# Performance work log

Hardware: AMD Instinct MI355X
Metric: run time of the kernel (lower is better)

Reference implementation:

```python
import jax, jax.numpy as jnp
import numpy as np

R = 4  # search_range

def setup_inputs() -> dict:
    key = jax.random.key(0)
    k1, k2 = jax.random.split(key)
    B, C, H, W = 4, 128, 96, 160
    src = jax.random.normal(k1, (B, C, H, W), dtype=jnp.float32)
    tgt = jax.random.normal(k2, (B, C, H, W), dtype=jnp.float32)
    return {"src": src, "tgt": tgt}

def _cost_volume(src, tgt):
    B, C, H, W = src.shape
    # zero-pad tgt by R on each spatial side (as in F.pad(tgt, [R]*4))
    tp = jnp.pad(tgt, ((0, 0), (0, 0), (R, R), (R, R)))
    # shifted map cropped to the central HxW window; shift (dh, dw) means
    # the neighbor at offset (dh, dw) relative to each src pixel.
    def crop(dh, dw):
        return tp[:, :, R + dh:R + dh + H, R + dw:R + dw + W]
    # order matches torch: [identity, left, right, up, down] for i=1..R
    maps = [crop(0, 0)]
    for i in range(1, R + 1):
        maps.extend([crop(-i, 0), crop(i, 0), crop(0, -i), crop(0, i)])
    neigh = jnp.stack(maps, axis=2)  # [B, C, 1+4R, H, W]
    # correlation: sum over channels -> [B, 1+4R, H, W]
    return jnp.einsum('bchw,bcshw->bshw', src, neigh)

def reference(src, tgt):
    return _cost_volume(src, tgt)
```

## Files before the change

kernel.cpp:

```cpp
#include <hip/hip_runtime.h>

#define RR 4
#define NS 17
#define BB 4
#define CC 128
#define HH 96
#define WW 160
#define HWSZ (HH * WW)

#define TW 32
#define HTILE 8
#define TROWS (HTILE + 2 * RR)
#define TCOLS (TW + 2 * RR)
#define TILE_E (TROWS * TCOLS)
#define CCHUNK 32
#define NCHUNK (CC / CCHUNK)
#define CG 4
#define NG (CCHUNK / CG)
#define NSPX (WW / TW)
#define NSPY (HH / HTILE)
#define NSP (NSPX * NSPY)
#define NWG (NSP * BB * NCHUNK)
#define NXCD 8
#define WGPX (NWG / NXCD)

#define FMA4(a, t) \
    (a) = fmaf(svx, (t).x, fmaf(svy, (t).y, fmaf(svz, (t).z, fmaf(svw, (t).w, (a)))))

__global__ __launch_bounds__(256, 4)
void cost_volume_kernel(const float* __restrict__ src,
                        const float* __restrict__ tgt,
                        float* __restrict__ out) {
    __shared__ float4 tile[TILE_E];

    const int x   = threadIdx.x;
    const int hg  = threadIdx.y;
    const int tid = hg * TW + x;

    const int flat = blockIdx.x;
    const int wg   = (flat & (NXCD - 1)) * WGPX + (flat >> 3);
    const int sp   = wg % NSP;
    const int z    = wg / NSP;
    const int wx   = sp % NSPX;
    const int wy   = sp / NSPX;

    const int w0 = wx * TW;
    const int h0 = wy * HTILE;
    const int b  = z & 3;
    const int c0 = (z >> 2) * CCHUNK;

    const int w = w0 + x;
    const int h = h0 + hg;

    const float* tgt_b = tgt + (size_t)(b * CC + c0) * HWSZ;
    const float* src_p = src + (size_t)(b * CC + c0) * HWSZ + h * WW + w;

    int  sOff[3];
    bool sVal[3];
#pragma unroll
    for (int k = 0; k < 3; ++k) {
        const int idx = tid + k * 256;
        const int r   = idx / TCOLS;
        const int col = idx - r * TCOLS;
        const int gr  = h0 - RR + r;
        const int gc  = w0 - RR + col;
        sVal[k] = (idx < TILE_E) && gr >= 0 && gr < HH && gc >= 0 && gc < WW;
        sOff[k] = gr * WW + gc;
    }

    float4 pre[3];
    float  sv4[4];

    auto fetch = [&](int g) {
        const float* t = tgt_b + (size_t)(g * CG) * HWSZ;
#pragma unroll
        for (int k = 0; k < 3; ++k) {
            float4 v = make_float4(0.f, 0.f, 0.f, 0.f);
            if (sVal[k]) {
                const float* p = t + sOff[k];
                v.x = p[0];
                v.y = p[HWSZ];
                v.z = p[2 * HWSZ];
                v.w = p[3 * HWSZ];
            }
            pre[k] = v;
        }
        const float* s = src_p + (size_t)(g * CG) * HWSZ;
#pragma unroll
        for (int k = 0; k < 4; ++k) sv4[k] = s[k * HWSZ];
    };

    float acc[NS];
#pragma unroll
    for (int s = 0; s < NS; ++s) acc[s] = 0.f;

    fetch(0);
    const int base = (RR + hg) * TCOLS + (RR + x);

    for (int g = 0; g < NG; ++g) {
        tile[tid]       = pre[0];
        tile[tid + 256] = pre[1];
        if (tid + 512 < TILE_E) tile[tid + 512] = pre[2];
        const float svx = sv4[0], svy = sv4[1], svz = sv4[2], svw = sv4[3];
        __syncthreads();

        if (g + 1 < NG) fetch(g + 1);

        {
            float4 tc = tile[base];
            FMA4(acc[0], tc);
#pragma unroll
            for (int off = 1; off <= RR; ++off) {
                float4 tu = tile[base - off * TCOLS];
                float4 td = tile[base + off * TCOLS];
                float4 tl = tile[base - off];
                float4 tr = tile[base + off];
                FMA4(acc[4 * off - 3], tu);
                FMA4(acc[4 * off - 2], td);
                FMA4(acc[4 * off - 1], tl);
                FMA4(acc[4 * off    ], tr);
            }
        }
        __syncthreads();
    }

    float* op = out + (((size_t)b * NS) * HH + h) * WW + w;
#pragma unroll
    for (int s = 0; s < NS; ++s) {
        atomicAdd(op + (size_t)s * HWSZ, acc[s]);
    }
}

extern "C" void kernel_launch(void* const* d_in, const int* in_sizes, int n_in,
                              void* d_out, int out_size, void* d_ws, size_t ws_size,
                              hipStream_t stream) {
    const float* src = (const float*)d_in[0];
    const float* tgt = (const float*)d_in[1];
    float* out = (float*)d_out;

    hipMemsetAsync(out, 0, (size_t)out_size * sizeof(float), stream);

    dim3 block(TW, 8, 1);
    dim3 grid(NWG, 1, 1);
    cost_volume_kernel<<<grid, block, 0, stream>>>(src, tgt, out);
}
```

Before: 107.4 us.

## Double-buffer shared tile and halve channel chunk for more workgroups

Switches the shared-memory tile to two buffers, so each channel group needs one barrier instead of two. The next group is stored into the alternate buffer after compute, and the loop is fully unrolled. The channel chunk per workgroup drops from 32 to 16, which doubles the grid and the number of atomic adds to the output. The launch-bounds occupancy hint rises to 6. Doubling LDS per block and adding atomic traffic may offset the gains in parallelism and synchronisation.

```diff
diff --git a/kernel.cpp b/kernel.cpp
--- a/kernel.cpp
+++ b/kernel.cpp
@@ -13,7 +13,7 @@
 #define TROWS (HTILE + 2 * RR)
 #define TCOLS (TW + 2 * RR)
 #define TILE_E (TROWS * TCOLS)
-#define CCHUNK 32
+#define CCHUNK 16
 #define NCHUNK (CC / CCHUNK)
 #define CG 4
 #define NG (CCHUNK / CG)
@@ -27,11 +27,11 @@
 #define FMA4(a, t) \
     (a) = fmaf(svx, (t).x, fmaf(svy, (t).y, fmaf(svz, (t).z, fmaf(svw, (t).w, (a)))))
 
-__global__ __launch_bounds__(256, 4)
+__global__ __launch_bounds__(256, 6)
 void cost_volume_kernel(const float* __restrict__ src,
                         const float* __restrict__ tgt,
                         float* __restrict__ out) {
-    __shared__ float4 tile[TILE_E];
+    __shared__ float4 tile[2][TILE_E];
 
     const int x   = threadIdx.x;
     const int hg  = threadIdx.y;
@@ -69,9 +69,10 @@
     }
 
     float4 pre[3];
-    float  sv4[4];
+    float  svc[4];
+    float  svn[4];
 
-    auto fetch = [&](int g) {
+    auto fetch = [&](int g, float sv[4]) {
         const float* t = tgt_b + (size_t)(g * CG) * HWSZ;
 #pragma unroll
         for (int k = 0; k < 3; ++k) {
@@ -87,41 +88,55 @@
         }
         const float* s = src_p + (size_t)(g * CG) * HWSZ;
 #pragma unroll
-        for (int k = 0; k < 4; ++k) sv4[k] = s[k * HWSZ];
+        for (int k = 0; k < 4; ++k) sv[k] = s[k * HWSZ];
+    };
+
+    auto store_tile = [&](int buf) {
+        tile[buf][tid]       = pre[0];
+        tile[buf][tid + 256] = pre[1];
+        if (tid + 512 < TILE_E) tile[buf][tid + 512] = pre[2];
     };
 
     float acc[NS];
 #pragma unroll
     for (int s = 0; s < NS; ++s) acc[s] = 0.f;
 
-    fetch(0);
+    fetch(0, svc);
+    store_tile(0);
+    __syncthreads();
+
     const int base = (RR + hg) * TCOLS + (RR + x);
 
+#pragma unroll
     for (int g = 0; g < NG; ++g) {
-        tile[tid]       = pre[0];
-        tile[tid + 256] = pre[1];
-        if (tid + 512 < TILE_E) tile[tid + 512] = pre[2];
-        const float svx = sv4[0], svy = sv4[1], svz = sv4[2], svw = sv4[3];
-        __syncthreads();
+        const int cur = g & 1;
 
-        if (g + 1 < NG) fetch(g + 1);
+        if (g + 1 < NG) fetch(g + 1, svn);
 
         {
-            float4 tc = tile[base];
+            const float svx = svc[0], svy = svc[1], svz = svc[2], svw = svc[3];
+            const float4* tb = tile[cur];
+            float4 tc = tb[base];
             FMA4(acc[0], tc);
 #pragma unroll
             for (int off = 1; off <= RR; ++off) {
-                float4 tu = tile[base - off * TCOLS];
-                float4 td = tile[base + off * TCOLS];
-                float4 tl = tile[base - off];
-                float4 tr = tile[base + off];
+                float4 tu = tb[base - off * TCOLS];
+                float4 td = tb[base + off * TCOLS];
+                float4 tl = tb[base - off];
+                float4 tr = tb[base + off];
                 FMA4(acc[4 * off - 3], tu);
                 FMA4(acc[4 * off - 2], td);
                 FMA4(acc[4 * off - 1], tl);
                 FMA4(acc[4 * off    ], tr);
             }
         }
-        __syncthreads();
+
+        if (g + 1 < NG) {
+            store_tile(cur ^ 1);
+#pragma unroll
+            for (int k = 0; k < 4; ++k) svc[k] = svn[k];
+            __syncthreads();
+        }
     }
 
     float* op = out + (((size_t)b * NS) * HH + h) * WW + w;
```

Result: slower. 243.7 us (+126.9%).

## Compute two output rows per thread to reuse vertical tile loads

Applied to the files above, without the earlier changes.

Each thread now computes two vertically adjacent output pixels, doubling the tile height to 16 rows. The shared-memory column of ten float4 values is loaded once and feeds both rows' vertical-shift accumulators, which cuts LDS reads per output and shrinks the halo overhead relative to the tile. The XCD-aware block remapping is replaced by a channel-major linear ordering. The cost is twice as many accumulator registers, which may pressure occupancy under the 4-waves launch bound, and half as many workgroups.

```diff
diff --git a/kernel.cpp b/kernel.cpp
--- a/kernel.cpp
+++ b/kernel.cpp
@@ -9,7 +9,8 @@
 #define HWSZ (HH * WW)
 
 #define TW 32
-#define HTILE 8
+#define HTILE 16
+#define TH 2
 #define TROWS (HTILE + 2 * RR)
 #define TCOLS (TW + 2 * RR)
 #define TILE_E (TROWS * TCOLS)
@@ -21,11 +22,9 @@
 #define NSPY (HH / HTILE)
 #define NSP (NSPX * NSPY)
 #define NWG (NSP * BB * NCHUNK)
-#define NXCD 8
-#define WGPX (NWG / NXCD)
 
-#define FMA4(a, t) \
-    (a) = fmaf(svx, (t).x, fmaf(svy, (t).y, fmaf(svz, (t).z, fmaf(svw, (t).w, (a)))))
+#define FMA4S(a, t, s0, s1, s2, s3) \
+    (a) = fmaf((s0), (t).x, fmaf((s1), (t).y, fmaf((s2), (t).z, fmaf((s3), (t).w, (a)))))
 
 __global__ __launch_bounds__(256, 4)
 void cost_volume_kernel(const float* __restrict__ src,
@@ -38,27 +37,27 @@
     const int tid = hg * TW + x;
 
     const int flat = blockIdx.x;
-    const int wg   = (flat & (NXCD - 1)) * WGPX + (flat >> 3);
-    const int sp   = wg % NSP;
-    const int z    = wg / NSP;
-    const int wx   = sp % NSPX;
-    const int wy   = sp / NSPX;
+    const int ch   = flat / 120;
+    const int rr_  = flat % 120;
+    const int b    = rr_ / NSP;
+    const int spl  = rr_ % NSP;
+    const int wx   = spl % NSPX;
+    const int wy   = spl / NSPX;
 
+    const int c0 = ch * CCHUNK;
     const int w0 = wx * TW;
     const int h0 = wy * HTILE;
-    const int b  = z & 3;
-    const int c0 = (z >> 2) * CCHUNK;
 
-    const int w = w0 + x;
-    const int h = h0 + hg;
+    const int w  = w0 + x;
+    const int hb = h0 + hg * TH;
 
     const float* tgt_b = tgt + (size_t)(b * CC + c0) * HWSZ;
-    const float* src_p = src + (size_t)(b * CC + c0) * HWSZ + h * WW + w;
+    const float* src_p = src + (size_t)(b * CC + c0) * HWSZ + hb * WW + w;
 
-    int  sOff[3];
-    bool sVal[3];
+    int  sOff[4];
+    bool sVal[4];
 #pragma unroll
-    for (int k = 0; k < 3; ++k) {
+    for (int k = 0; k < 4; ++k) {
         const int idx = tid + k * 256;
         const int r   = idx / TCOLS;
         const int col = idx - r * TCOLS;
@@ -68,13 +67,13 @@
         sOff[k] = gr * WW + gc;
     }
 
-    float4 pre[3];
-    float  sv4[4];
+    float4 pre[4];
+    float  sv[2][4];
 
     auto fetch = [&](int g) {
         const float* t = tgt_b + (size_t)(g * CG) * HWSZ;
 #pragma unroll
-        for (int k = 0; k < 3; ++k) {
+        for (int k = 0; k < 4; ++k) {
             float4 v = make_float4(0.f, 0.f, 0.f, 0.f);
             if (sVal[k]) {
                 const float* p = t + sOff[k];
@@ -87,47 +86,64 @@
         }
         const float* s = src_p + (size_t)(g * CG) * HWSZ;
 #pragma unroll
-        for (int k = 0; k < 4; ++k) sv4[k] = s[k * HWSZ];
+        for (int k = 0; k < 4; ++k) {
+            sv[0][k] = s[k * HWSZ];
+            sv[1][k] = s[k * HWSZ + WW];
+        }
     };
 
-    float acc[NS];
+    float acc0[NS], acc1[NS];
 #pragma unroll
-    for (int s = 0; s < NS; ++s) acc[s] = 0.f;
+    for (int s = 0; s < NS; ++s) { acc0[s] = 0.f; acc1[s] = 0.f; }
 
     fetch(0);
-    const int base = (RR + hg) * TCOLS + (RR + x);
+    const int tr0 = RR + hg * TH;
+    const int cc  = RR + x;
 
     for (int g = 0; g < NG; ++g) {
         tile[tid]       = pre[0];
         tile[tid + 256] = pre[1];
-        if (tid + 512 < TILE_E) tile[tid + 512] = pre[2];
-        const float svx = sv4[0], svy = sv4[1], svz = sv4[2], svw = sv4[3];
+        tile[tid + 512] = pre[2];
+        if (tid < TILE_E - 768) tile[tid + 768] = pre[3];
+        const float a0 = sv[0][0], a1 = sv[0][1], a2 = sv[0][2], a3 = sv[0][3];
+        const float b0 = sv[1][0], b1 = sv[1][1], b2 = sv[1][2], b3 = sv[1][3];
         __syncthreads();
 
         if (g + 1 < NG) fetch(g + 1);
 
-        {
-            float4 tc = tile[base];
-            FMA4(acc[0], tc);
 #pragma unroll
-            for (int off = 1; off <= RR; ++off) {
-                float4 tu = tile[base - off * TCOLS];
-                float4 td = tile[base + off * TCOLS];
-                float4 tl = tile[base - off];
-                float4 tr = tile[base + off];
-                FMA4(acc[4 * off - 3], tu);
-                FMA4(acc[4 * off - 2], td);
-                FMA4(acc[4 * off - 1], tl);
-                FMA4(acc[4 * off    ], tr);
+        for (int j = 0; j < 10; ++j) {
+            float4 v = tile[(tr0 - RR + j) * TCOLS + cc];
+            if (j <= 8) {
+                if (j == 4)      FMA4S(acc0[0],             v, a0, a1, a2, a3);
+                else if (j < 4)  FMA4S(acc0[4 * (4 - j) - 3], v, a0, a1, a2, a3);
+                else             FMA4S(acc0[4 * (j - 4) - 2], v, a0, a1, a2, a3);
             }
+            if (j >= 1) {
+                if (j == 5)      FMA4S(acc1[0],             v, b0, b1, b2, b3);
+                else if (j < 5)  FMA4S(acc1[4 * (5 - j) - 3], v, b0, b1, b2, b3);
+                else             FMA4S(acc1[4 * (j - 5) - 2], v, b0, b1, b2, b3);
+            }
+        }
+#pragma unroll
+        for (int off = 1; off <= RR; ++off) {
+            float4 l0 = tile[tr0 * TCOLS + cc - off];
+            float4 r0 = tile[tr0 * TCOLS + cc + off];
+            float4 l1 = tile[(tr0 + 1) * TCOLS + cc - off];
+            float4 r1 = tile[(tr0 + 1) * TCOLS + cc + off];
+            FMA4S(acc0[4 * off - 1], l0, a0, a1, a2, a3);
+            FMA4S(acc0[4 * off    ], r0, a0, a1, a2, a3);
+            FMA4S(acc1[4 * off - 1], l1, b0, b1, b2, b3);
+            FMA4S(acc1[4 * off    ], r1, b0, b1, b2, b3);
         }
         __syncthreads();
     }
 
-    float* op = out + (((size_t)b * NS) * HH + h) * WW + w;
+    float* op = out + (((size_t)b * NS) * HH + hb) * WW + w;
 #pragma unroll
     for (int s = 0; s < NS; ++s) {
-        atomicAdd(op + (size_t)s * HWSZ, acc[s]);
+        atomicAdd(op + (size_t)s * HWSZ, acc0[s]);
+        atomicAdd(op + (size_t)s * HWSZ + WW, acc1[s]);
     }
 }
 
```

New measurement: 303.0 us. 2.82x slower.
